# Kernel tuning notes

Hardware: AMD Instinct MI355X
Metric: run time of the kernel (lower is better)

Reference implementation:

```python
import jax, jax.numpy as jnp
import numpy as np

B, N, E = 128, 1024, 16384
ENTITY, EMB, HID = 100000, 100, 100


def setup_inputs() -> dict:
    key = jax.random.key(0)
    ks = jax.random.split(key, 13)
    s = 0.1  # param init scale
    return {
        "neighbors": jax.random.randint(ks[0], (B, N), 0, ENTITY),
        "adj_row": jax.random.randint(ks[1], (B, E), 0, N),
        "adj_col": jax.random.randint(ks[2], (B, E), 0, N),
        "adj_val": jax.random.uniform(ks[3], (B, E), jnp.float32),
        "emb_table": jax.random.normal(ks[4], (ENTITY, EMB), jnp.float32) * s,
        "gcn_w": jax.random.normal(ks[5], (EMB, HID), jnp.float32) * s,
        "gcn_b": jax.random.normal(ks[6], (HID,), jnp.float32) * s,
        "w_ih": jax.random.normal(ks[7], (3 * HID, HID), jnp.float32) * s,
        "w_hh": jax.random.normal(ks[8], (3 * HID, HID), jnp.float32) * s,
        "b_ih": jax.random.normal(ks[9], (3 * HID,), jnp.float32) * s,
        "b_hh": jax.random.normal(ks[10], (3 * HID,), jnp.float32) * s,
        "fc1_w": jax.random.normal(ks[11], (HID, HID), jnp.float32) * s,
        "fc1_b": jax.random.normal(ks[12], (HID,), jnp.float32) * s,
    }


def reference(neighbors, adj_row, adj_col, adj_val, emb_table,
              gcn_w, gcn_b, w_ih, w_hh, b_ih, b_hh, fc1_w, fc1_b):
    n_nodes = neighbors.shape[1]
    # Embedding lookup: [B, N, EMB]
    x = emb_table[neighbors]
    # GCN layer: support = X @ W, then sparse adj @ support, then + bias
    support = jnp.einsum('bne,eh->bnh', x, gcn_w)  # [B, N, HID]

    def spmm(row, col, val, sup):
        # out[r] += val * sup[col]  (per-sample sparse aggregation)
        return jax.ops.segment_sum(val[:, None] * sup[col], row,
                                   num_segments=n_nodes)

    seq = jax.vmap(spmm)(adj_row, adj_col, adj_val, support) + gcn_b  # [B,N,HID]

    # GRU over node sequence (PyTorch gate order: r, z, n)
    def gru_step(h, x_t):
        gx = x_t @ w_ih.T + b_ih
        gh = h @ w_hh.T + b_hh
        xr, xz, xn = jnp.split(gx, 3, axis=-1)
        hr, hz, hn = jnp.split(gh, 3, axis=-1)
        r = jax.nn.sigmoid(xr + hr)
        z = jax.nn.sigmoid(xz + hz)
        n = jnp.tanh(xn + r * hn)
        h_new = (1.0 - z) * n + z * h
        return h_new, None

    h0 = jnp.zeros((seq.shape[0], w_hh.shape[1]), seq.dtype)
    h, _ = jax.lax.scan(gru_step, h0, seq.transpose(1, 0, 2))  # final hidden [B,HID]

    # h.permute(1,0,2) -> [B, 1, HID], then relu(fc1(.))
    return jax.nn.relu(h[:, None, :] @ fc1_w.T + fc1_b)
```

## Files before the change

kernel.cpp:

```cpp
#include <hip/hip_runtime.h>
#include <hip/hip_bf16.h>


typedef unsigned int u32;
typedef float f2 __attribute__((ext_vector_type(2)));

__device__ __forceinline__ float bflo(u32 u) {
    union { u32 i; float f; } v; v.i = u << 16; return v.f;
}
__device__ __forceinline__ float bfhi(u32 u) {
    union { u32 i; float f; } v; v.i = u & 0xffff0000u; return v.f;
}
__device__ __forceinline__ u32 f2bf1(float f) {
    union { float f; u32 u; } v; v.f = f;
    return (v.u + 0x7fffu + ((v.u >> 16) & 1u)) >> 16;
}
__device__ __forceinline__ u32 packbf(float a, float b) {
    return f2bf1(a) | (f2bf1(b) << 16);
}
__device__ __forceinline__ float sigm(float x) { return 1.f / (1.f + __expf(-x)); }
__device__ __forceinline__ float tanh_fast(float x) {
    float e = __expf(2.f * x);
    return 1.f - 2.f / (e + 1.f);
}

__global__ __launch_bounds__(256, 2)
void gcn_kernel(const int* __restrict__ nb, const float* __restrict__ emb,
                const float* __restrict__ w, u32* __restrict__ support)
{
    __shared__ float wl[10000];
    for (int i = threadIdx.x; i < 10000; i += 256) wl[i] = w[i];
    __syncthreads();

    const int n = blockIdx.x * 256 + threadIdx.x;
    const long long row = nb[n];
    const float4* __restrict__ xr = (const float4*)(emb + row * 100);

    float acc[100];
#pragma unroll
    for (int h = 0; h < 100; ++h) acc[h] = 0.f;

    for (int kk = 0; kk < 25; ++kk) {
        const float4 xv = xr[kk];
        const float xs[4] = { xv.x, xv.y, xv.z, xv.w };
#pragma unroll
        for (int q = 0; q < 4; ++q) {
            const float* wrow = &wl[(kk * 4 + q) * 100];
            const float xq = xs[q];
#pragma unroll
            for (int h4 = 0; h4 < 25; ++h4) {
                const float4 w4 = *(const float4*)(wrow + h4 * 4);
                acc[h4*4+0] = fmaf(xq, w4.x, acc[h4*4+0]);
                acc[h4*4+1] = fmaf(xq, w4.y, acc[h4*4+1]);
                acc[h4*4+2] = fmaf(xq, w4.z, acc[h4*4+2]);
                acc[h4*4+3] = fmaf(xq, w4.w, acc[h4*4+3]);
            }
        }
    }

    u32* __restrict__ o = support + (size_t)n * 50;
#pragma unroll
    for (int i = 0; i < 50; ++i) o[i] = packbf(acc[2*i], acc[2*i+1]);
}

__global__ __launch_bounds__(256, 2)
void csr_build(const int* __restrict__ arow, const int* __restrict__ acol,
               const float* __restrict__ aval,
               int* __restrict__ offs, int2* __restrict__ csr)
{
    __shared__ int cnt[1024];
    __shared__ int part[256];
    __shared__ int offl[1024];

    const int b   = blockIdx.x;
    const int tid = threadIdx.x;
    const int*   rw = arow + b * 16384;
    const int*   cl = acol + b * 16384;
    const float* vl = aval + b * 16384;

    for (int i = tid; i < 1024; i += 256) cnt[i] = 0;
    __syncthreads();
    for (int e = tid; e < 16384; e += 256) atomicAdd(&cnt[rw[e]], 1);
    __syncthreads();

    int c[4]; int s = 0;
#pragma unroll
    for (int q = 0; q < 4; ++q) { c[q] = cnt[tid * 4 + q]; s += c[q]; }
    part[tid] = s;
    __syncthreads();
    for (int off = 1; off < 256; off <<= 1) {
        int v = (tid >= off) ? part[tid - off] : 0;
        __syncthreads();
        part[tid] += v;
        __syncthreads();
    }
    int run = part[tid] - s;
#pragma unroll
    for (int q = 0; q < 4; ++q) { offl[tid * 4 + q] = run; run += c[q]; }
    __syncthreads();

    for (int i = tid; i < 1024; i += 256) offs[b * 1025 + i] = offl[i];
    if (tid == 0) offs[b * 1025 + 1024] = 16384;

    int2* cs = csr + (size_t)b * 16384;
    for (int e = tid; e < 16384; e += 256) {
        const int r   = rw[e];
        const int pos = atomicAdd(&offl[r], 1);
        int2 cv; cv.x = cl[e]; cv.y = __float_as_int(vl[e]);
        cs[pos] = cv;
    }
}

__global__ __launch_bounds__(256, 4)
void spmm_agg(const int* __restrict__ offs, const int2* __restrict__ csr,
              const u32* __restrict__ support,
              const float* __restrict__ gcn_b, u32* __restrict__ seq)
{
    const int b    = blockIdx.y;
    const int lr   = threadIdx.x / 50;
    const int lane = threadIdx.x % 50;
    const int r    = blockIdx.x * 5 + lr;
    if (lr >= 5 || r >= 1024) return;

    const int e0 = offs[b * 1025 + r];
    const int e1 = offs[b * 1025 + r + 1];
    const int2* __restrict__ cs = csr + (size_t)b * 16384;
    const u32* __restrict__ supb = support + (size_t)b * 1024 * 50;

    float a0 = 0.f, a1 = 0.f;
    for (int e = e0; e < e1; ++e) {
        const int2 cv = cs[e];
        const float v = __int_as_float(cv.y);
        const u32 u = supb[(size_t)cv.x * 50 + lane];
        a0 = fmaf(v, bflo(u), a0);
        a1 = fmaf(v, bfhi(u), a1);
    }
    a0 += gcn_b[2 * lane];
    a1 += gcn_b[2 * lane + 1];
    seq[((size_t)b * 1024 + r) * 50 + lane] = packbf(a0, a1);
}

__global__ __launch_bounds__(256, 2)
void gx_gemm0(const u32* __restrict__ seq, const float* __restrict__ w_ih,
              const float* __restrict__ b_ih, u32* __restrict__ gxW,
              int c0, int ctl, int CT)
{
    __shared__ float wl[10000];
    const int g    = blockIdx.x % 3;
    const int tile = blockIdx.x / 3;
    const int tid  = threadIdx.x;

    for (int i = tid; i < 10000; i += 256)
        wl[(i % 100) * 100 + (i / 100)] = w_ih[g * 10000 + i];
    __syncthreads();

    const int m = tile * 256 + tid;
    const int b = m >> ctl;
    const int t = m & (CT - 1);
    const uint2* sr2 = (const uint2*)(seq + ((size_t)b * 1024 + c0 + t) * 50);

    float acc[100];
    const float4* bi4 = (const float4*)(b_ih + g * 100);
#pragma unroll
    for (int j4 = 0; j4 < 25; ++j4) {
        const float4 bv = bi4[j4];
        acc[j4*4+0] = bv.x; acc[j4*4+1] = bv.y; acc[j4*4+2] = bv.z; acc[j4*4+3] = bv.w;
    }

    for (int kk = 0; kk < 25; ++kk) {
        const uint2 up = sr2[kk];
        const float xs[4] = { bflo(up.x), bfhi(up.x), bflo(up.y), bfhi(up.y) };
#pragma unroll
        for (int q = 0; q < 4; ++q) {
            const float* wrow = &wl[(kk * 4 + q) * 100];
            const float xq = xs[q];
#pragma unroll
            for (int j4 = 0; j4 < 25; ++j4) {
                const float4 w4 = *(const float4*)(wrow + j4 * 4);
                acc[j4*4+0] = fmaf(xq, w4.x, acc[j4*4+0]);
                acc[j4*4+1] = fmaf(xq, w4.y, acc[j4*4+1]);
                acc[j4*4+2] = fmaf(xq, w4.z, acc[j4*4+2]);
                acc[j4*4+3] = fmaf(xq, w4.w, acc[j4*4+3]);
            }
        }
    }

    u32* og = gxW + (size_t)m * 150 + g * 50;
#pragma unroll
    for (int i = 0; i < 50; ++i) og[i] = packbf(acc[2*i], acc[2*i+1]);
}

__global__ __launch_bounds__(512, 2)
void gru_v7(const u32* __restrict__ gxR, size_t sampStride,
            const float* __restrict__ w_hh, const float* __restrict__ b_hh,
            float* __restrict__ hg, const float* __restrict__ fc1_w,
            const float* __restrict__ fc1_b, float* __restrict__ out,
            int first, int last, int CT)
{
    __shared__ float hb[2][112];

    const int tid  = threadIdx.x;
    const int samp = blockIdx.x;
    const int j    = tid >> 2;
    const int p    = tid & 3;
    const int hi   = j & 1;
    const int jc   = (j < 100) ? j : 99;

#define WDECL(g) f2 g##0a, g##0b, g##1a, g##1b, g##2a, g##2b, g##3a, g##3b, \
                    g##4a, g##4b, g##5a, g##5b, g##6a, g##6b
    WDECL(wr); WDECL(wz); WDECL(wn);
#undef WDECL

    {
        const float* r0 = w_hh + (size_t)jc * 100;
#define WLOAD(i)                                                              \
        {                                                                     \
            const int   q  = 4 * (i) + p;                                     \
            const int   qc = (q < 25) ? q : 24;                               \
            const float mm = (q < 25) ? 1.f : 0.f;                            \
            float4 v;                                                         \
            v = *(const float4*)(r0 + 4 * qc);                                \
            wr##i##a = (f2){v.x * mm, v.y * mm};                              \
            wr##i##b = (f2){v.z * mm, v.w * mm};                              \
            v = *(const float4*)(r0 + 10000 + 4 * qc);                        \
            wz##i##a = (f2){v.x * mm, v.y * mm};                              \
            wz##i##b = (f2){v.z * mm, v.w * mm};                              \
            v = *(const float4*)(r0 + 20000 + 4 * qc);                        \
            wn##i##a = (f2){v.x * mm, v.y * mm};                              \
            wn##i##b = (f2){v.z * mm, v.w * mm};                              \
        }
        WLOAD(0) WLOAD(1) WLOAD(2) WLOAD(3) WLOAD(4) WLOAD(5) WLOAD(6)
#undef WLOAD
    }

    const float bhr = b_hh[jc];
    const float bhz = b_hh[100 + jc];
    const float bhn = b_hh[200 + jc];
    float hreg = first ? 0.f : hg[samp * 100 + jc];

    if (j < 100 && p == 0) hb[0][j] = hreg;
    if (tid >= 100 && tid < 112) { hb[0][tid] = 0.f; hb[1][tid] = 0.f; }
    __syncthreads();

    const int w50 = ((j >> 1) < 50) ? (j >> 1) : 49;
    const u32* gp = gxR + (size_t)samp * sampStride + w50;
    u32 a0 = gp[0],   a1 = gp[50],  a2 = gp[100];
    u32 b0 = gp[150], b1 = gp[200], b2 = gp[250];

    int cur = 0;

#define SG(i)                                                                 \
    {                                                                         \
        const float4 hv = *(const float4*)(hc + 16 * (i));                    \
        const f2 h01 = {hv.x, hv.y}, h23 = {hv.z, hv.w};                      \
        ar0 += wr##i##a * h01;  ar1 += wr##i##b * h23;                        \
        az0 += wz##i##a * h01;  az1 += wz##i##b * h23;                        \
        an0 += wn##i##a * h01;  an1 += wn##i##b * h23;                        \
    }

#define GRU_STEP(T, X0, X1, X2)                                               \
    {                                                                         \
        const float* hc = &hb[cur][4 * p];                                    \
        f2 ar0 = {0.f,0.f}, ar1 = {0.f,0.f};                                  \
        f2 az0 = {0.f,0.f}, az1 = {0.f,0.f};                                  \
        f2 an0 = {0.f,0.f}, an1 = {0.f,0.f};                                  \
        SG(0) SG(1) SG(2) SG(3) SG(4) SG(5) SG(6)                             \
        const u32 c0 = X0, c1 = X1, c2 = X2;                                  \
        if ((T) + 2 < CT) {                                                   \
            const u32* q2 = gp + (size_t)((T) + 2) * 150;                     \
            X0 = q2[0]; X1 = q2[50]; X2 = q2[100];                            \
        }                                                                     \
        float sr = (ar0.x + ar0.y) + (ar1.x + ar1.y);                         \
        float sz = (az0.x + az0.y) + (az1.x + az1.y);                         \
        float sn = (an0.x + an0.y) + (an1.x + an1.y);                         \
        sr += __shfl_xor(sr, 1);  sz += __shfl_xor(sz, 1);                    \
        sn += __shfl_xor(sn, 1);                                              \
        sr += __shfl_xor(sr, 2);  sz += __shfl_xor(sz, 2);                    \
        sn += __shfl_xor(sn, 2);                                              \
        const float gxr = hi ? bfhi(c0) : bflo(c0);                           \
        const float gxz = hi ? bfhi(c1) : bflo(c1);                           \
        const float gxn = hi ? bfhi(c2) : bflo(c2);                           \
        const float rg  = sigm(gxr + sr + bhr);                               \
        const float zg  = sigm(gxz + sz + bhz);                               \
        const float ng  = tanh_fast(gxn + rg * (sn + bhn));                   \
        hreg = (1.f - zg) * ng + zg * hreg;                                   \
        if (j < 100 && p == 0) hb[cur ^ 1][j] = hreg;                         \
        __syncthreads();                                                      \
        cur ^= 1;                                                             \
    }

    for (int t = 0; t < CT; t += 2) {
        GRU_STEP(t,     a0, a1, a2);
        GRU_STEP(t + 1, b0, b1, b2);
    }
#undef GRU_STEP
#undef SG

    if (j < 100 && p == 0) hg[samp * 100 + j] = hreg;
    if (last && tid < 100) {
        const float* hc = hb[cur];
        const float4* fw = (const float4*)(fc1_w + (size_t)tid * 100);
        float s0 = 0.f, s1 = 0.f, s2 = 0.f, s3 = 0.f;
#pragma unroll
        for (int kk = 0; kk < 25; ++kk) {
            const float4 wv = fw[kk];
            const float4 hv = *(const float4*)(hc + kk * 4);
            s0 = fmaf(wv.x, hv.x, s0);
            s1 = fmaf(wv.y, hv.y, s1);
            s2 = fmaf(wv.z, hv.z, s2);
            s3 = fmaf(wv.w, hv.w, s3);
        }
        const float s = (s0 + s1) + (s2 + s3) + fc1_b[tid];
        out[samp * 100 + tid] = fmaxf(s, 0.f);
    }
}

extern "C" void kernel_launch(void* const* d_in, const int* in_sizes, int n_in,
                              void* d_out, int out_size, void* d_ws, size_t ws_size,
                              hipStream_t stream)
{
    const int*   neighbors = (const int*)  d_in[0];
    const int*   adj_row   = (const int*)  d_in[1];
    const int*   adj_col   = (const int*)  d_in[2];
    const float* adj_val   = (const float*)d_in[3];
    const float* emb       = (const float*)d_in[4];
    const float* gcn_w     = (const float*)d_in[5];
    const float* gcn_b     = (const float*)d_in[6];
    const float* w_ih      = (const float*)d_in[7];
    const float* w_hh      = (const float*)d_in[8];
    const float* b_ih      = (const float*)d_in[9];
    const float* b_hh      = (const float*)d_in[10];
    const float* fc1_w     = (const float*)d_in[11];
    const float* fc1_b     = (const float*)d_in[12];
    float* out = (float*)d_out;

    char* ws = (char*)d_ws;
    const size_t seq_bytes     = (size_t)128 * 1024 * 50 * 4;
    const size_t hg_bytes      = 128 * 100 * 4;
    const size_t support_bytes = (size_t)128 * 1024 * 50 * 4;
    const size_t offs_bytes    = (size_t)128 * 1025 * 4;

    u32*   seq = (u32*)ws;
    float* hg  = (float*)(ws + seq_bytes);
    char*  rest = ws + seq_bytes + hg_bytes;
    const size_t rest_avail = ws_size - seq_bytes - hg_bytes;

    u32*  support = (u32*)rest;
    int*  offs    = (int*)(rest + support_bytes);
    int2* csr     = (int2*)(rest + support_bytes + offs_bytes);

    gcn_kernel<<<512, 256, 0, stream>>>(neighbors, emb, gcn_w, support);
    csr_build<<<128, 256, 0, stream>>>(adj_row, adj_col, adj_val, offs, csr);
    spmm_agg<<<dim3(205, 128), 256, 0, stream>>>(offs, csr, support, gcn_b, seq);

    const size_t gx_full = (size_t)128 * 1024 * 150 * 4;
    u32* gx = (u32*)rest;

    if (rest_avail >= gx_full) {
        gx_gemm0<<<1536, 256, 0, stream>>>(seq, w_ih, b_ih, gx, 0, 10, 1024);
        gru_v7<<<128, 512, 0, stream>>>(gx, (size_t)1024 * 150, w_hh, b_hh, hg,
                                        fc1_w, fc1_b, out, 1, 1, 1024);
    } else {
        int CT = 512, ctl = 9;
        while (CT > 8 && (size_t)128 * CT * 150 * 4 > rest_avail) { CT >>= 1; --ctl; }
        const int nch = 1024 / CT;
        for (int c = 0; c < nch; ++c) {
            gx_gemm0<<<3 * (128 * CT / 256), 256, 0, stream>>>(seq, w_ih, b_ih, gx,
                                                               c * CT, ctl, CT);
            gru_v7<<<128, 512, 0, stream>>>(gx, (size_t)CT * 150, w_hh, b_hh, hg,
                                            fc1_w, fc1_b, out,
                                            (c == 0) ? 1 : 0, (c == nch - 1) ? 1 : 0, CT);
        }
    }
}
```

Baseline: 1.326 ms.

## Halve GRU threads per hidden unit and hold W_hh as packed bf16

```diff
diff --git a/kernel.cpp b/kernel.cpp
--- a/kernel.cpp
+++ b/kernel.cpp
@@ -190,46 +190,48 @@
     for (int i = 0; i < 50; ++i) og[i] = packbf(acc[2*i], acc[2*i+1]);
 }
 
-__global__ __launch_bounds__(512, 2)
-void gru_v7(const u32* __restrict__ gxR, size_t sampStride,
-            const float* __restrict__ w_hh, const float* __restrict__ b_hh,
-            float* __restrict__ hg, const float* __restrict__ fc1_w,
-            const float* __restrict__ fc1_b, float* __restrict__ out,
-            int first, int last, int CT)
-{
-    __shared__ float hb[2][112];
+__global__ __launch_bounds__(256, 1)
+void gru_v12(const u32* __restrict__ gxR, size_t sampStride,
+             const float* __restrict__ w_hh, const float* __restrict__ b_hh,
+             float* __restrict__ hg, const float* __restrict__ fc1_w,
+             const float* __restrict__ fc1_b, float* __restrict__ out,
+             int first, int last, int CT)
+{
+    __shared__ float hb[2][104];
 
     const int tid  = threadIdx.x;
     const int samp = blockIdx.x;
-    const int j    = tid >> 2;
-    const int p    = tid & 3;
+    const int j    = tid >> 1;
+    const int p    = tid & 1;
     const int hi   = j & 1;
     const int jc   = (j < 100) ? j : 99;
 
-#define WDECL(g) f2 g##0a, g##0b, g##1a, g##1b, g##2a, g##2b, g##3a, g##3b, \
-                    g##4a, g##4b, g##5a, g##5b, g##6a, g##6b
+#define WDECL(g) u32 g##0a, g##0b, g##1a, g##1b, g##2a, g##2b, g##3a, g##3b,  \
+                     g##4a, g##4b, g##5a, g##5b, g##6a, g##6b, g##7a, g##7b,  \
+                     g##8a, g##8b, g##9a, g##9b, g##10a, g##10b, g##11a,      \
+                     g##11b, g##12a, g##12b
     WDECL(wr); WDECL(wz); WDECL(wn);
 #undef WDECL
-
     {
         const float* r0 = w_hh + (size_t)jc * 100;
 #define WLOAD(i)                                                              \
         {                                                                     \
-            const int   q  = 4 * (i) + p;                                     \
+            const int   q  = 2 * (i) + p;                                     \
             const int   qc = (q < 25) ? q : 24;                               \
             const float mm = (q < 25) ? 1.f : 0.f;                            \
             float4 v;                                                         \
             v = *(const float4*)(r0 + 4 * qc);                                \
-            wr##i##a = (f2){v.x * mm, v.y * mm};                              \
-            wr##i##b = (f2){v.z * mm, v.w * mm};                              \
+            wr##i##a = packbf(v.x * mm, v.y * mm);                            \
+            wr##i##b = packbf(v.z * mm, v.w * mm);                            \
             v = *(const float4*)(r0 + 10000 + 4 * qc);                        \
-            wz##i##a = (f2){v.x * mm, v.y * mm};                              \
-            wz##i##b = (f2){v.z * mm, v.w * mm};                              \
+            wz##i##a = packbf(v.x * mm, v.y * mm);                            \
+            wz##i##b = packbf(v.z * mm, v.w * mm);                            \
             v = *(const float4*)(r0 + 20000 + 4 * qc);                        \
-            wn##i##a = (f2){v.x * mm, v.y * mm};                              \
-            wn##i##b = (f2){v.z * mm, v.w * mm};                              \
+            wn##i##a = packbf(v.x * mm, v.y * mm);                            \
+            wn##i##b = packbf(v.z * mm, v.w * mm);                            \
         }
         WLOAD(0) WLOAD(1) WLOAD(2) WLOAD(3) WLOAD(4) WLOAD(5) WLOAD(6)
+        WLOAD(7) WLOAD(8) WLOAD(9) WLOAD(10) WLOAD(11) WLOAD(12)
 #undef WLOAD
     }
 
@@ -238,11 +240,11 @@
     const float bhn = b_hh[200 + jc];
     float hreg = first ? 0.f : hg[samp * 100 + jc];
 
-    if (j < 100 && p == 0) hb[0][j] = hreg;
-    if (tid >= 100 && tid < 112) { hb[0][tid] = 0.f; hb[1][tid] = 0.f; }
-    __syncthreads();
-
-    const int w50 = ((j >> 1) < 50) ? (j >> 1) : 49;
+    if (tid < 200 && p == 0) hb[0][j] = hreg;
+    if (tid >= 100 && tid < 104) { hb[0][tid] = 0.f; hb[1][tid] = 0.f; }
+    __syncthreads();
+
+    const int w50 = ((tid >> 2) < 50) ? (tid >> 2) : 49;
     const u32* gp = gxR + (size_t)samp * sampStride + w50;
     u32 a0 = gp[0],   a1 = gp[50],  a2 = gp[100];
     u32 b0 = gp[150], b1 = gp[200], b2 = gp[250];
@@ -251,11 +253,17 @@
 
 #define SG(i)                                                                 \
     {                                                                         \
-        const float4 hv = *(const float4*)(hc + 16 * (i));                    \
+        const float4 hv = *(const float4*)(hc + 8 * (i));                     \
         const f2 h01 = {hv.x, hv.y}, h23 = {hv.z, hv.w};                      \
-        ar0 += wr##i##a * h01;  ar1 += wr##i##b * h23;                        \
-        az0 += wz##i##a * h01;  az1 += wz##i##b * h23;                        \
-        an0 += wn##i##a * h01;  an1 += wn##i##b * h23;                        \
+        const f2 wra = {bflo(wr##i##a), bfhi(wr##i##a)};                      \
+        const f2 wrb = {bflo(wr##i##b), bfhi(wr##i##b)};                      \
+        ar0 += wra * h01;  ar1 += wrb * h23;                                  \
+        const f2 wza = {bflo(wz##i##a), bfhi(wz##i##a)};                      \
+        const f2 wzb = {bflo(wz##i##b), bfhi(wz##i##b)};                      \
+        az0 += wza * h01;  az1 += wzb * h23;                                  \
+        const f2 wna = {bflo(wn##i##a), bfhi(wn##i##a)};                      \
+        const f2 wnb = {bflo(wn##i##b), bfhi(wn##i##b)};                      \
+        an0 += wna * h01;  an1 += wnb * h23;                                  \
     }
 
 #define GRU_STEP(T, X0, X1, X2)                                               \
@@ -265,6 +273,7 @@
         f2 az0 = {0.f,0.f}, az1 = {0.f,0.f};                                  \
         f2 an0 = {0.f,0.f}, an1 = {0.f,0.f};                                  \
         SG(0) SG(1) SG(2) SG(3) SG(4) SG(5) SG(6)                             \
+        SG(7) SG(8) SG(9) SG(10) SG(11) SG(12)                                \
         const u32 c0 = X0, c1 = X1, c2 = X2;                                  \
         if ((T) + 2 < CT) {                                                   \
             const u32* q2 = gp + (size_t)((T) + 2) * 150;                     \
@@ -273,10 +282,9 @@
         float sr = (ar0.x + ar0.y) + (ar1.x + ar1.y);                         \
         float sz = (az0.x + az0.y) + (az1.x + az1.y);                         \
         float sn = (an0.x + an0.y) + (an1.x + an1.y);                         \
-        sr += __shfl_xor(sr, 1);  sz += __shfl_xor(sz, 1);                    \
+        sr += __shfl_xor(sr, 1);                                              \
+        sz += __shfl_xor(sz, 1);                                              \
         sn += __shfl_xor(sn, 1);                                              \
-        sr += __shfl_xor(sr, 2);  sz += __shfl_xor(sz, 2);                    \
-        sn += __shfl_xor(sn, 2);                                              \
         const float gxr = hi ? bfhi(c0) : bflo(c0);                           \
         const float gxz = hi ? bfhi(c1) : bflo(c1);                           \
         const float gxn = hi ? bfhi(c2) : bflo(c2);                           \
@@ -284,7 +292,7 @@
         const float zg  = sigm(gxz + sz + bhz);                               \
         const float ng  = tanh_fast(gxn + rg * (sn + bhn));                   \
         hreg = (1.f - zg) * ng + zg * hreg;                                   \
-        if (j < 100 && p == 0) hb[cur ^ 1][j] = hreg;                         \
+        if (tid < 200 && p == 0) hb[cur ^ 1][j] = hreg;                       \
         __syncthreads();                                                      \
         cur ^= 1;                                                             \
     }
@@ -296,7 +304,7 @@
 #undef GRU_STEP
 #undef SG
 
-    if (j < 100 && p == 0) hg[samp * 100 + j] = hreg;
+    if (tid < 200 && p == 0) hg[samp * 100 + j] = hreg;
     if (last && tid < 100) {
         const float* hc = hb[cur];
         const float4* fw = (const float4*)(fc1_w + (size_t)tid * 100);
@@ -358,8 +366,8 @@
 
     if (rest_avail >= gx_full) {
         gx_gemm0<<<1536, 256, 0, stream>>>(seq, w_ih, b_ih, gx, 0, 10, 1024);
-        gru_v7<<<128, 512, 0, stream>>>(gx, (size_t)1024 * 150, w_hh, b_hh, hg,
-                                        fc1_w, fc1_b, out, 1, 1, 1024);
+        gru_v12<<<128, 256, 0, stream>>>(gx, (size_t)1024 * 150, w_hh, b_hh, hg,
+                                         fc1_w, fc1_b, out, 1, 1, 1024);
     } else {
         int CT = 512, ctl = 9;
         while (CT > 8 && (size_t)128 * CT * 150 * 4 > rest_avail) { CT >>= 1; --ctl; }
@@ -367,9 +375,9 @@
         for (int c = 0; c < nch; ++c) {
             gx_gemm0<<<3 * (128 * CT / 256), 256, 0, stream>>>(seq, w_ih, b_ih, gx,
                                                                c * CT, ctl, CT);
-            gru_v7<<<128, 512, 0, stream>>>(gx, (size_t)CT * 150, w_hh, b_hh, hg,
-                                            fc1_w, fc1_b, out,
-                                            (c == 0) ? 1 : 0, (c == nch - 1) ? 1 : 0, CT);
-        }
-    }
-}
+            gru_v12<<<128, 256, 0, stream>>>(gx, (size_t)CT * 150, w_hh, b_hh, hg,
+                                             fc1_w, fc1_b, out,
+                                             (c == 0) ? 1 : 0, (c == nch - 1) ? 1 : 0, CT);
+        }
+    }
+}
```

After: 1.167 ms. 1.14x faster.
